# Optimization experiments

Hardware: AMD Instinct MI355X
Metric: run time of the kernel (lower is better)

## Reference

```python
import jax, jax.numpy as jnp
import numpy as np

B, N, D, H = 64, 64, 128, 256
DIN = N + 4        # z_where(2) + one-hot(N) + actions(2)
DOUT = 2
TAU = 0.5
BN_EPS = 1e-5
KL_EPS = 1e-16


def mlp_bn(x, w1, b1, g, bb, w2, b2):
    # Linear -> ReLU -> BatchNorm1d (training mode, stats over all leading dims) -> Linear
    h = jax.nn.relu(jnp.einsum('...i,ih->...h', x, w1) + b1)
    hf = h.reshape(-1, h.shape[-1])
    mu = hf.mean(0)
    var = hf.var(0)  # biased variance, as torch BN uses for normalization
    h = (h - mu) * jax.lax.rsqrt(var + BN_EPS) * g + bb
    return jnp.einsum('...h,ho->...o', h, w2) + b2


def setup_inputs():
    key = jax.random.key(0)
    ks = jax.random.split(key, 16)
    def W(k, i, o):
        return jax.random.normal(k, (i, o), jnp.float32) / np.float32(np.sqrt(i))
    u = jax.random.uniform(ks[0], (B, N, N, 2), jnp.float32, 1e-10, 1.0 - 1e-10)
    gumbel_noise = -jnp.log(-jnp.log(u))
    z = jnp.zeros
    return {
        'states': jax.random.normal(ks[1], (B, N, D), jnp.float32),
        'z_where': jax.random.normal(ks[2], (B, N, 2), jnp.float32),
        'actions': jax.random.normal(ks[3], (B, 2), jnp.float32),
        'gumbel_noise': gumbel_noise,
        'self_w1': W(ks[4], DIN, H), 'self_b1': z((H,)), 'self_g': jnp.ones((H,)), 'self_bb': z((H,)),
        'self_w2': W(ks[5], H, D), 'self_b2': z((D,)),
        'rel_w1': W(ks[6], 2 * D, H), 'rel_b1': z((H,)), 'rel_g': jnp.ones((H,)), 'rel_bb': z((H,)),
        'rel_w2': W(ks[7], H, D), 'rel_b2': z((D,)),
        'wgt_w1': W(ks[8], 2 * D, H), 'wgt_b1': z((H,)), 'wgt_g': jnp.ones((H,)), 'wgt_bb': z((H,)),
        'wgt_w2': W(ks[9], H, 2), 'wgt_b2': z((2,)),
        'pred_w1': W(ks[10], D, H), 'pred_b1': z((H,)), 'pred_g': jnp.ones((H,)), 'pred_bb': z((H,)),
        'pred_w2': W(ks[11], H, DOUT), 'pred_b2': z((DOUT,)),
        'gru_wih': W(ks[12], 2 * D, 3 * D), 'gru_whh': W(ks[13], D, 3 * D),
        'gru_bih': z((3 * D,)), 'gru_bhh': z((3 * D,)),
    }


def prop_gt_forward(states, z_where, actions, gumbel_noise,
                    self_w1, self_b1, self_g, self_bb, self_w2, self_b2,
                    rel_w1, rel_b1, rel_g, rel_bb, rel_w2, rel_b2,
                    wgt_w1, wgt_b1, wgt_g, wgt_bb, wgt_w2, wgt_b2,
                    pred_w1, pred_b1, pred_g, pred_bb, pred_w2, pred_b2,
                    gru_wih, gru_whh, gru_bih, gru_bhh):
    b = states.shape[0]
    eye = jnp.eye(N, dtype=states.dtype)
    # feat = [z_where, one-hot id, broadcast action] : (B, N, DIN)
    z_what = jnp.broadcast_to(eye[None], (b, N, N))
    act = jnp.broadcast_to(actions[:, None, :], (b, N, 2))
    feat = jnp.concatenate([z_where, z_what, act], axis=-1)
    enc_self = mlp_bn(feat, self_w1, self_b1, self_g, self_bb, self_w2, self_b2)  # (B,N,D)

    # recurrent dynamics: pairwise state concat (B, N, N, 2D)
    s_self = jnp.broadcast_to(states[:, :, None, :], (b, N, N, D))
    s_other = jnp.broadcast_to(states[:, None, :, :], (b, N, N, D))
    feat_matrix = jnp.concatenate([s_self, s_other], axis=-1)

    relational = mlp_bn(feat_matrix, rel_w1, rel_b1, rel_g, rel_bb, rel_w2, rel_b2)  # (B,N,N,D)
    logits = mlp_bn(feat_matrix, wgt_w1, wgt_b1, wgt_g, wgt_bb, wgt_w2, wgt_b2)      # (B,N,N,2)

    # gumbel-softmax, hard with straight-through
    y_soft = jax.nn.softmax((logits + gumbel_noise) / TAU, axis=-1)
    y_hard = jax.nn.one_hot(jnp.argmax(y_soft, axis=-1), 2, dtype=y_soft.dtype)
    y = jax.lax.stop_gradient(y_hard - y_soft) + y_soft
    weight = y[..., 0:1]  # (B,N,N,1)

    # KL(prob || prior) as in NRI
    log_prior = jnp.log(jnp.array([0.05, 0.95], dtype=logits.dtype))
    prob = jax.nn.softmax(logits, axis=-1)
    kl_loss = jnp.sum(prob * (jnp.log(prob + KL_EPS) - log_prior)) / (N * b)

    # self mask: zero diagonal edges
    weight = weight * (1.0 - eye)[None, :, :, None]

    enc_rel = jnp.sum(weight * relational, axis=2)  # (B,N,D)

    # TrackerRNN: GRU cell update of states with [enc_self, enc_rel]
    x = jnp.concatenate([enc_self, enc_rel], axis=-1)  # (B,N,2D)
    gi = jnp.einsum('bni,ih->bnh', x, gru_wih) + gru_bih
    gh = jnp.einsum('bnd,dh->bnh', states, gru_whh) + gru_bhh
    gi_r, gi_z, gi_n = jnp.split(gi, 3, axis=-1)
    gh_r, gh_z, gh_n = jnp.split(gh, 3, axis=-1)
    r = jax.nn.sigmoid(gi_r + gh_r)
    zg = jax.nn.sigmoid(gi_z + gh_z)
    n = jnp.tanh(gi_n + r * gh_n)
    updated_state = (1.0 - zg) * n + zg * states  # (B,N,D)

    z_where_next = mlp_bn(updated_state, pred_w1, pred_b1, pred_g, pred_bb, pred_w2, pred_b2)
    return (updated_state, z_where_next.reshape(b, -1), weight, kl_loss)


def reference(states, z_where, actions, gumbel_noise,
              self_w1, self_b1, self_g, self_bb, self_w2, self_b2,
              rel_w1, rel_b1, rel_g, rel_bb, rel_w2, rel_b2,
              wgt_w1, wgt_b1, wgt_g, wgt_bb, wgt_w2, wgt_b2,
              pred_w1, pred_b1, pred_g, pred_bb, pred_w2, pred_b2,
              gru_wih, gru_whh, gru_bih, gru_bhh):
    return prop_gt_forward(states, z_where, actions, gumbel_noise,
                           self_w1, self_b1, self_g, self_bb, self_w2, self_b2,
                           rel_w1, rel_b1, rel_g, rel_bb, rel_w2, rel_b2,
                           wgt_w1, wgt_b1, wgt_g, wgt_bb, wgt_w2, wgt_b2,
                           pred_w1, pred_b1, pred_g, pred_bb, pred_w2, pred_b2,
                           gru_wih, gru_whh, gru_bih, gru_bhh)
```

## Files before the change

kernel.cpp:

```cpp
#include <hip/hip_runtime.h>
#include <math.h>

#define BATCH 64
#define NOBJ  64
#define DDIM  128
#define HDIM  256
#define ROWS  (BATCH*NOBJ)
#define PAIRS (ROWS*NOBJ)

#define OFF_A_REL    (0ull)
#define OFF_B_REL    (4ull<<20)
#define OFF_A_WGT    (8ull<<20)
#define OFF_B_WGT    (12ull<<20)
#define OFF_BWT      (16ull<<20)
#define OFF_H_SELF   (20ull<<20)
#define OFF_ENC_SELF (24ull<<20)
#define OFF_ENC_REL  (26ull<<20)
#define OFF_H_PRED   (28ull<<20)
#define OFF_STATS    (32ull<<20)
#define OFF_KLP      (OFF_STATS + 16384)
#define OFF_W2P      (OFF_STATS + 65536)
#define OFF_C2       (OFF_W2P + 128*1024)
#define OFF_W2PD     (OFF_C2 + 512)
#define OFF_C2W      (OFF_W2PD + 4096)
#define OFF_SW2P     (OFF_C2W + 256)
#define OFF_SC2      (OFF_SW2P + 128*1024)

#define OUT_UPD 0
#define OUT_ZWN (ROWS*DDIM)
#define OUT_WGT (OUT_ZWN + ROWS*2)
#define OUT_KL  (OUT_WGT + PAIRS)

__global__ __launch_bounds__(256) void k_pre(
    const float* __restrict__ states,
    const float* __restrict__ rel_w1, const float* __restrict__ rel_b1,
    const float* __restrict__ wgt_w1, const float* __restrict__ wgt_b1,
    const float* __restrict__ z_where, const float* __restrict__ actions,
    const float* __restrict__ self_w1, const float* __restrict__ self_b1,
    float* __restrict__ A_rel, float* __restrict__ B_rel,
    float* __restrict__ A_wgt, float* __restrict__ B_wgt,
    float* __restrict__ B_wgtT, float* __restrict__ h_self,
    double* __restrict__ stats)
{
    const int t = threadIdx.x;
    const int view = blockIdx.y;
    const int row0 = blockIdx.x * 16;

    if (view == 4) {
        const float w_zw0 = self_w1[0*256+t], w_zw1 = self_w1[1*256+t];
        const float w_a0  = self_w1[66*256+t], w_a1 = self_w1[67*256+t];
        const float bb1 = self_b1[t];
        double sum = 0.0, ssq = 0.0;
        for (int r = 0; r < 16; ++r) {
            const int row = row0 + r;
            const int b = row >> 6, i = row & 63;
            const float zw0 = z_where[row*2], zw1 = z_where[row*2+1];
            const float a0 = actions[b*2], a1 = actions[b*2+1];
            float v = self_w1[(2+i)*256+t] + bb1;
            v = fmaf(zw0, w_zw0, v); v = fmaf(zw1, w_zw1, v);
            v = fmaf(a0, w_a0, v);   v = fmaf(a1, w_a1, v);
            v = fmaxf(v, 0.f);
            h_self[row*256+t] = v;
            sum += (double)v; ssq = fma((double)v, (double)v, ssq);
        }
        atomicAdd(&stats[4*256+t], sum);
        atomicAdd(&stats[5*256+t], ssq);
        return;
    }

    __shared__ float s_tile[16][128];
    for (int f4 = t; f4 < 512; f4 += 256)
        *(float4*)&s_tile[0][f4*4] = *(const float4*)&states[row0*128 + f4*4];
    __syncthreads();

    const float* wbase = (view == 0) ? rel_w1
                       : (view == 1) ? rel_w1 + 128*256
                       : (view == 2) ? wgt_w1
                       :               wgt_w1 + 128*256;
    const float* wp = wbase + t;
    float acc[16];
#pragma unroll
    for (int r = 0; r < 16; ++r) acc[r] = 0.f;
#pragma unroll 4
    for (int k = 0; k < 128; ++k) {
        const float wv = wp[k*256];
#pragma unroll
        for (int r = 0; r < 16; ++r) acc[r] = fmaf(s_tile[r][k], wv, acc[r]);
    }

    if (view == 0) {
        const float bias = rel_b1[t];
#pragma unroll
        for (int r = 0; r < 16; ++r) A_rel[(row0+r)*256 + t] = acc[r] + bias;
    } else if (view == 1) {
#pragma unroll
        for (int r = 0; r < 16; ++r) B_rel[(row0+r)*256 + t] = acc[r];
    } else if (view == 2) {
        const float bias = wgt_b1[t];
#pragma unroll
        for (int r = 0; r < 16; ++r) A_wgt[(row0+r)*256 + t] = acc[r] + bias;
    } else {
#pragma unroll
        for (int r = 0; r < 16; ++r) B_wgt[(row0+r)*256 + t] = acc[r];
        const int b = row0 >> 6, j0 = row0 & 63;
        float* bt = &B_wgtT[((size_t)b*256 + t)*64 + j0];
        *(float4*)(bt+0)  = make_float4(acc[0],  acc[1],  acc[2],  acc[3]);
        *(float4*)(bt+4)  = make_float4(acc[4],  acc[5],  acc[6],  acc[7]);
        *(float4*)(bt+8)  = make_float4(acc[8],  acc[9],  acc[10], acc[11]);
        *(float4*)(bt+12) = make_float4(acc[12], acc[13], acc[14], acc[15]);
    }
}

__global__ __launch_bounds__(256) void k_bn_stats(
    const float* __restrict__ A_rel, const float* __restrict__ B_rel,
    const float* __restrict__ A_wgt, const float* __restrict__ B_wgt,
    double* __restrict__ stats)
{
    const int h = threadIdx.x;
    const int b = blockIdx.y, i0 = blockIdx.x * 8;
    float ar[8], aw[8];
#pragma unroll
    for (int r = 0; r < 8; ++r) {
        ar[r] = A_rel[(b*64 + i0 + r)*256 + h];
        aw[r] = A_wgt[(b*64 + i0 + r)*256 + h];
    }
    float  srel0 = 0.f, ssrel0 = 0.f, srel1 = 0.f, ssrel1 = 0.f;
    double swgt = 0.0, sswgt = 0.0;
    for (int j = 0; j < 64; j += 2) {
        const float br0 = B_rel[(b*64+j)*256 + h];
        const float bw0 = B_wgt[(b*64+j)*256 + h];
        const float br1 = B_rel[(b*64+j+1)*256 + h];
        const float bw1 = B_wgt[(b*64+j+1)*256 + h];
#pragma unroll
        for (int r = 0; r < 8; ++r) {
            const float v0 = fmaxf(ar[r] + br0, 0.f);
            srel0 += v0; ssrel0 = fmaf(v0, v0, ssrel0);
            const float vw0 = fmaxf(aw[r] + bw0, 0.f);
            swgt += (double)vw0; sswgt = fma((double)vw0, (double)vw0, sswgt);
        }
#pragma unroll
        for (int r = 0; r < 8; ++r) {
            const float v1 = fmaxf(ar[r] + br1, 0.f);
            srel1 += v1; ssrel1 = fmaf(v1, v1, ssrel1);
            const float vw1 = fmaxf(aw[r] + bw1, 0.f);
            swgt += (double)vw1; sswgt = fma((double)vw1, (double)vw1, sswgt);
        }
    }
    atomicAdd(&stats[0*256+h], (double)(srel0 + srel1));
    atomicAdd(&stats[1*256+h], (double)(ssrel0 + ssrel1));
    atomicAdd(&stats[2*256+h], swgt);
    atomicAdd(&stats[3*256+h], sswgt);
}

__global__ __launch_bounds__(256) void k_finalize(
    const double* __restrict__ stats,
    const float* __restrict__ rel_g, const float* __restrict__ rel_bb,
    const float* __restrict__ rel_w2, const float* __restrict__ rel_b2,
    const float* __restrict__ wgt_g, const float* __restrict__ wgt_bb,
    const float* __restrict__ wgt_w2, const float* __restrict__ wgt_b2,
    const float* __restrict__ self_g, const float* __restrict__ self_bb,
    const float* __restrict__ self_w2, const float* __restrict__ self_b2,
    float* __restrict__ W2p, float* __restrict__ c2,
    double* __restrict__ W2pd, double* __restrict__ c2w,
    float* __restrict__ sW2p, float* __restrict__ sc2)
{
    __shared__ float  rscale[256], rshift[256], sscale[256], sshift[256];
    __shared__ double wshift[256];
    const int k = threadIdx.x;
    {
        const double cnt = 262144.0;
        double mu  = stats[0*256+k]/cnt;
        double var = stats[1*256+k]/cnt - mu*mu;
        float  sc  = (float)((double)rel_g[k] / sqrt(var + 1e-5));
        rscale[k] = sc;
        rshift[k] = rel_bb[k] - (float)mu * sc;
        double muw  = stats[2*256+k]/cnt;
        double varw = stats[3*256+k]/cnt - muw*muw;
        double scw  = (double)wgt_g[k] / sqrt(varw + 1e-5);
        wshift[k]   = (double)wgt_bb[k] - muw*scw;
        if (blockIdx.x == 0) {
            W2pd[2*k]   = scw * (double)wgt_w2[2*k];
            W2pd[2*k+1] = scw * (double)wgt_w2[2*k+1];
        }
        const double cnts = 4096.0;
        double mus  = stats[4*256+k]/cnts;
        double vars = stats[5*256+k]/cnts - mus*mus;
        float  scs  = (float)((double)self_g[k] / sqrt(vars + 1e-5));
        sscale[k] = scs;
        sshift[k] = self_bb[k] - (float)mus*scs;
    }
    __syncthreads();
    const int base = blockIdx.x * 8192;
    for (int idx = base + k; idx < base + 8192; idx += 256) {
        const int kk = idx >> 7;
        W2p[idx]  = rscale[kk]*rel_w2[idx];
        sW2p[idx] = sscale[kk]*self_w2[idx];
    }
    if (blockIdx.x == 0) {
        if (k < 128) {
            float acc = rel_b2[k], accs = self_b2[k];
            for (int kk = 0; kk < 256; ++kk) {
                acc  = fmaf(rshift[kk], rel_w2[kk*128+k], acc);
                accs = fmaf(sshift[kk], self_w2[kk*128+k], accs);
            }
            c2[k] = acc; sc2[k] = accs;
        }
        if (k < 2) {
            double acc = (double)wgt_b2[k];
            for (int kk = 0; kk < 256; ++kk) acc += wshift[kk]*(double)wgt_w2[kk*2+k];
            c2w[k] = acc;
        }
    }
}

__global__ __launch_bounds__(256) void k_main(
    const float* __restrict__ A_rel, const float* __restrict__ B_rel,
    const float* __restrict__ A_wgt, const float* __restrict__ B_wgtT,
    const double* __restrict__ W2pd, const double* __restrict__ c2w,
    const float* __restrict__ gumbel,
    const float* __restrict__ W2p, const float* __restrict__ c2,
    float* __restrict__ enc_rel, float* __restrict__ weight_out,
    float* __restrict__ klp)
{
    __shared__ float  a_lds[4][256];
    __shared__ double w2_lds[512];
    __shared__ double red0[4][4][64], red1[4][4][64];
    __shared__ float  w_lds[4][64];
    __shared__ float  klred[256];
    __shared__ float  h_lds[4][256];
    __shared__ float  redf[4][256];
    const int t = threadIdx.x;
    const int blk = blockIdx.x;
    const int row0 = blk * 4;
    const int b = row0 >> 6;

    w2_lds[t]     = W2pd[t];
    w2_lds[256+t] = W2pd[256+t];
    float a_rel[4];
#pragma unroll
    for (int r = 0; r < 4; ++r) {
        a_lds[r][t] = A_wgt[(row0+r)*256 + t];
        a_rel[r]    = A_rel[(row0+r)*256 + t];
    }
    __syncthreads();

    {
        const int j = t & 63, q = t >> 6;
        double acc0[4] = {0,0,0,0}, acc1[4] = {0,0,0,0};
        const float* btp = &B_wgtT[((size_t)b*256 + q*64)*64 + j];
#pragma unroll 4
        for (int kk = 0; kk < 64; ++kk) {
            const int k = q*64 + kk;
            const float  bw = btp[kk*64];
            const double w0 = w2_lds[2*k], w1 = w2_lds[2*k+1];
#pragma unroll
            for (int r = 0; r < 4; ++r) {
                const double hw = (double)fmaxf(a_lds[r][k] + bw, 0.f);
                acc0[r] = fma(hw, w0, acc0[r]);
                acc1[r] = fma(hw, w1, acc1[r]);
            }
        }
#pragma unroll
        for (int r = 0; r < 4; ++r) { red0[r][q][j] = acc0[r]; red1[r][q][j] = acc1[r]; }
    }
    __syncthreads();

    {
        const int r = t >> 6, j = t & 63;
        const double l0 = red0[r][0][j]+red0[r][1][j]+red0[r][2][j]+red0[r][3][j] + c2w[0];
        const double l1 = red1[r][0][j]+red1[r][1][j]+red1[r][2][j]+red1[r][3][j] + c2w[1];
        const int row = row0 + r;
        const float g0 = gumbel[(row*64+j)*2], g1 = gumbel[(row*64+j)*2+1];
        float w = (l0 + (double)g0 >= l1 + (double)g1) ? 1.f : 0.f;
        if (j == (row & 63)) w = 0.f;
        w_lds[r][j] = w;
        weight_out[row*64 + j] = w;
        const float lf0 = (float)l0, lf1 = (float)l1;
        const float m = fmaxf(lf0, lf1);
        const float e0 = expf(lf0 - m), e1 = expf(lf1 - m);
        const float s = e0 + e1;
        const float p0 = e0/s, p1 = e1/s;
        const float lp0 = -2.9957323f;
        const float lp1 = -0.05129329f;
        klred[t] = p0*(logf(p0+1e-16f) - lp0) + p1*(logf(p1+1e-16f) - lp1);
    }
    __syncthreads();
    if (t < 64) {
        float s = klred[t] + klred[t+64] + klred[t+128] + klred[t+192];
        for (int off = 32; off; off >>= 1) s += __shfl_down(s, off);
        if (t == 0) klp[blk] = s;
    }

    float sumw[4] = {0,0,0,0};
    {
        float g[4] = {0,0,0,0};
#pragma unroll 4
        for (int j = 0; j < 64; ++j) {
            const float br = B_rel[(b*64+j)*256 + t];
#pragma unroll
            for (int r = 0; r < 4; ++r) {
                const float w = w_lds[r][j];
                sumw[r] += w;
                g[r] = fmaf(w, fmaxf(a_rel[r] + br, 0.f), g[r]);
            }
        }
#pragma unroll
        for (int r = 0; r < 4; ++r) h_lds[r][t] = g[r];
    }
    __syncthreads();
    {
        const int d = t & 127, half = t >> 7;
        float acc[4] = {0,0,0,0};
        const float* wp = &W2p[half*128*128 + d];
#pragma unroll 2
        for (int kk = 0; kk < 128; ++kk) {
            const float wv = wp[kk*128];
#pragma unroll
            for (int r = 0; r < 4; ++r)
                acc[r] = fmaf(h_lds[r][half*128 + kk], wv, acc[r]);
        }
#pragma unroll
        for (int r = 0; r < 4; ++r) redf[r][t] = acc[r];
    }
    __syncthreads();
    if (t < 128) {
#pragma unroll
        for (int r = 0; r < 4; ++r)
            enc_rel[(row0+r)*128 + t] = redf[r][t] + redf[r][t+128] + sumw[r]*c2[t];
    }
}

__global__ __launch_bounds__(256) void k_enc_self(
    const float* __restrict__ h_self, const float* __restrict__ sW2p,
    const float* __restrict__ sc2, float* __restrict__ enc_self)
{
    __shared__ float h_lds[16*256];
    const int t = threadIdx.x;
    const int row0 = blockIdx.x * 16;
    for (int f4 = t; f4 < 1024; f4 += 256)
        *(float4*)&h_lds[f4*4] = *(const float4*)&h_self[row0*256 + f4*4];
    __syncthreads();
    const int d = t & 127, half = t >> 7;
    float acc[16];
#pragma unroll
    for (int r = 0; r < 16; ++r) acc[r] = 0.f;
    for (int kk = 0; kk < 128; ++kk) {
        const int k = half*128 + kk;
        const float wv = sW2p[k*128 + d];
#pragma unroll
        for (int r = 0; r < 16; ++r) acc[r] = fmaf(h_lds[r*256 + k], wv, acc[r]);
    }
    __syncthreads();
#pragma unroll
    for (int r = 0; r < 16; ++r) h_lds[r*256 + t] = acc[r];
    __syncthreads();
    for (int idx = t; idx < 16*128; idx += 256) {
        const int r = idx >> 7, dd = idx & 127;
        enc_self[(row0+r)*128 + dd] = h_lds[r*256 + dd] + h_lds[r*256 + 128 + dd] + sc2[dd];
    }
}

__global__ __launch_bounds__(384) void k_gru(
    const float* __restrict__ enc_self, const float* __restrict__ enc_rel,
    const float* __restrict__ states,
    const float* __restrict__ wih, const float* __restrict__ whh,
    const float* __restrict__ bih, const float* __restrict__ bhh,
    float* __restrict__ updated)
{
    __shared__ float x_lds[8][256];
    __shared__ float s_lds[8][128];
    __shared__ float gi_lds[8][384];
    __shared__ float gh_lds[8][384];
    const int t = threadIdx.x;
    const int row0 = blockIdx.x * 8;
    for (int idx = t; idx < 8*256; idx += 384) {
        const int r = idx >> 8, k = idx & 255;
        x_lds[r][k] = (k < 128) ? enc_self[(row0+r)*128 + k]
                                : enc_rel[(row0+r)*128 + (k-128)];
    }
    for (int idx = t; idx < 8*128; idx += 384) {
        const int r = idx >> 7, k = idx & 127;
        s_lds[r][k] = states[(row0+r)*128 + k];
    }
    __syncthreads();
    float gi[8], gh[8];
    const float bi = bih[t], bh = bhh[t];
#pragma unroll
    for (int r = 0; r < 8; ++r) { gi[r] = bi; gh[r] = bh; }
    for (int k = 0; k < 256; ++k) {
        const float w = wih[k*384 + t];
#pragma unroll
        for (int r = 0; r < 8; ++r) gi[r] = fmaf(x_lds[r][k], w, gi[r]);
    }
    for (int k = 0; k < 128; ++k) {
        const float w = whh[k*384 + t];
#pragma unroll
        for (int r = 0; r < 8; ++r) gh[r] = fmaf(s_lds[r][k], w, gh[r]);
    }
#pragma unroll
    for (int r = 0; r < 8; ++r) { gi_lds[r][t] = gi[r]; gh_lds[r][t] = gh[r]; }
    __syncthreads();
    for (int idx = t; idx < 8*128; idx += 384) {
        const int r = idx >> 7, d = idx & 127;
        const float gr = gi_lds[r][d]       + gh_lds[r][d];
        const float gz = gi_lds[r][128+d]   + gh_lds[r][128+d];
        const float rr = 1.f/(1.f + expf(-gr));
        const float zz = 1.f/(1.f + expf(-gz));
        const float nn = tanhf(gi_lds[r][256+d] + rr*gh_lds[r][256+d]);
        updated[(row0+r)*128 + d] = (1.f - zz)*nn + zz*s_lds[r][d];
    }
}

__global__ __launch_bounds__(256) void k_pred_h(
    const float* __restrict__ updated, const float* __restrict__ w1,
    const float* __restrict__ b1, float* __restrict__ h_pred,
    double* __restrict__ stats)
{
    __shared__ float u_lds[16][128];
    const int h = threadIdx.x;
    const int row0 = blockIdx.x * 16;
    for (int f4 = h; f4 < 512; f4 += 256)
        *(float4*)&u_lds[0][f4*4] = *(const float4*)&updated[row0*128 + f4*4];
    __syncthreads();
    float acc[16];
    const float bb1 = b1[h];
#pragma unroll
    for (int r = 0; r < 16; ++r) acc[r] = bb1;
#pragma unroll 4
    for (int k = 0; k < 128; ++k) {
        const float w = w1[k*256 + h];
#pragma unroll
        for (int r = 0; r < 16; ++r) acc[r] = fmaf(u_lds[r][k], w, acc[r]);
    }
    double sum = 0.0, ssq = 0.0;
#pragma unroll
    for (int r = 0; r < 16; ++r) {
        const float v = fmaxf(acc[r], 0.f);
        h_pred[(row0+r)*256 + h] = v;
        sum += (double)v; ssq = fma((double)v, (double)v, ssq);
    }
    atomicAdd(&stats[6*256+h], sum);
    atomicAdd(&stats[7*256+h], ssq);
}

__global__ __launch_bounds__(256) void k_pred_out(
    const float* __restrict__ h_pred, const double* __restrict__ stats,
    const float* __restrict__ g, const float* __restrict__ bbv,
    const float* __restrict__ w2, const float* __restrict__ b2,
    const float* __restrict__ klp,
    float* __restrict__ out_zw, float* __restrict__ out_kl)
{
    __shared__ float scale_lds[256], shift_lds[256];
    __shared__ float h_lds[32*256];
    __shared__ float red0[256], red1[256];
    __shared__ double kred[4];
    const int t = threadIdx.x;
    {
        const double mu  = stats[6*256+t]/4096.0;
        const double var = stats[7*256+t]/4096.0 - mu*mu;
        const float  sc  = (float)((double)g[t]/sqrt(var + 1e-5));
        scale_lds[t] = sc;
        shift_lds[t] = bbv[t] - (float)mu*sc;
    }
    const int row0 = blockIdx.x * 32;
    for (int idx = t; idx < 32*256; idx += 256)
        h_lds[idx] = h_pred[row0*256 + idx];
    __syncthreads();
    const int rl = t >> 3, q = t & 7;
    float a0 = 0.f, a1 = 0.f;
    for (int kk = 0; kk < 32; ++kk) {
        const int k = q*32 + kk;
        const float hn = fmaf(h_lds[rl*256 + k], scale_lds[k], shift_lds[k]);
        a0 = fmaf(hn, w2[k*2],   a0);
        a1 = fmaf(hn, w2[k*2+1], a1);
    }
    red0[t] = a0; red1[t] = a1;
    __syncthreads();
    if (t < 32) {
        float z0 = b2[0], z1 = b2[1];
        for (int q2 = 0; q2 < 8; ++q2) { z0 += red0[t*8+q2]; z1 += red1[t*8+q2]; }
        out_zw[(row0+t)*2]   = z0;
        out_zw[(row0+t)*2+1] = z1;
    }
    if (blockIdx.x == 0) {
        double s = 0.0;
        for (int idx = t; idx < 1024; idx += 256) s += (double)klp[idx];
        for (int off = 32; off; off >>= 1) s += __shfl_down(s, off);
        if ((t & 63) == 0) kred[t >> 6] = s;
        __syncthreads();
        if (t == 0)
            out_kl[0] = (float)((kred[0]+kred[1]+kred[2]+kred[3]) / 4096.0);
    }
}

extern "C" void kernel_launch(void* const* d_in, const int* in_sizes, int n_in,
                              void* d_out, int out_size, void* d_ws, size_t ws_size,
                              hipStream_t stream) {
    const float* states   = (const float*)d_in[0];
    const float* z_where  = (const float*)d_in[1];
    const float* actions  = (const float*)d_in[2];
    const float* gumbel   = (const float*)d_in[3];
    const float* self_w1  = (const float*)d_in[4];
    const float* self_b1  = (const float*)d_in[5];
    const float* self_g   = (const float*)d_in[6];
    const float* self_bb  = (const float*)d_in[7];
    const float* self_w2  = (const float*)d_in[8];
    const float* self_b2  = (const float*)d_in[9];
    const float* rel_w1   = (const float*)d_in[10];
    const float* rel_b1   = (const float*)d_in[11];
    const float* rel_g    = (const float*)d_in[12];
    const float* rel_bb   = (const float*)d_in[13];
    const float* rel_w2   = (const float*)d_in[14];
    const float* rel_b2   = (const float*)d_in[15];
    const float* wgt_w1   = (const float*)d_in[16];
    const float* wgt_b1   = (const float*)d_in[17];
    const float* wgt_g    = (const float*)d_in[18];
    const float* wgt_bb   = (const float*)d_in[19];
    const float* wgt_w2   = (const float*)d_in[20];
    const float* wgt_b2   = (const float*)d_in[21];
    const float* pred_w1  = (const float*)d_in[22];
    const float* pred_b1  = (const float*)d_in[23];
    const float* pred_g   = (const float*)d_in[24];
    const float* pred_bb  = (const float*)d_in[25];
    const float* pred_w2  = (const float*)d_in[26];
    const float* pred_b2  = (const float*)d_in[27];
    const float* gru_wih  = (const float*)d_in[28];
    const float* gru_whh  = (const float*)d_in[29];
    const float* gru_bih  = (const float*)d_in[30];
    const float* gru_bhh  = (const float*)d_in[31];

    char* ws = (char*)d_ws;
    float*  A_rel  = (float*) (ws + OFF_A_REL);
    float*  B_rel  = (float*) (ws + OFF_B_REL);
    float*  A_wgt  = (float*) (ws + OFF_A_WGT);
    float*  B_wgt  = (float*) (ws + OFF_B_WGT);
    float*  B_wgtT = (float*) (ws + OFF_BWT);
    float*  h_self = (float*) (ws + OFF_H_SELF);
    float*  encS   = (float*) (ws + OFF_ENC_SELF);
    float*  encR   = (float*) (ws + OFF_ENC_REL);
    float*  h_pred = (float*) (ws + OFF_H_PRED);
    double* stats  = (double*)(ws + OFF_STATS);
    float*  klp    = (float*) (ws + OFF_KLP);
    float*  W2p    = (float*) (ws + OFF_W2P);
    float*  c2     = (float*) (ws + OFF_C2);
    double* W2pd   = (double*)(ws + OFF_W2PD);
    double* c2w    = (double*)(ws + OFF_C2W);
    float*  sW2p   = (float*) (ws + OFF_SW2P);
    float*  sc2    = (float*) (ws + OFF_SC2);

    float* out = (float*)d_out;

    hipMemsetAsync(ws + OFF_STATS, 0, 8*256*8, stream);

    k_pre<<<dim3(256, 5), 256, 0, stream>>>(states, rel_w1, rel_b1, wgt_w1, wgt_b1,
                                            z_where, actions, self_w1, self_b1,
                                            A_rel, B_rel, A_wgt, B_wgt, B_wgtT,
                                            h_self, stats);
    k_bn_stats<<<dim3(8, 64), 256, 0, stream>>>(A_rel, B_rel, A_wgt, B_wgt, stats);
    k_finalize<<<4, 256, 0, stream>>>(stats, rel_g, rel_bb, rel_w2, rel_b2,
                                      wgt_g, wgt_bb, wgt_w2, wgt_b2,
                                      self_g, self_bb, self_w2, self_b2,
                                      W2p, c2, W2pd, c2w, sW2p, sc2);
    k_main<<<1024, 256, 0, stream>>>(A_rel, B_rel, A_wgt, B_wgtT, W2pd, c2w,
                                     gumbel, W2p, c2, encR, out + OUT_WGT, klp);
    k_enc_self<<<256, 256, 0, stream>>>(h_self, sW2p, sc2, encS);
    k_gru<<<512, 384, 0, stream>>>(encS, encR, states, gru_wih, gru_whh,
                                   gru_bih, gru_bhh, out + OUT_UPD);
    k_pred_h<<<256, 256, 0, stream>>>(out + OUT_UPD, pred_w1, pred_b1, h_pred, stats);
    k_pred_out<<<128, 256, 0, stream>>>(h_pred, stats, pred_g, pred_bb, pred_w2, pred_b2,
                                        klp, out + OUT_ZWN, out + OUT_KL);
}
```

Before: 202.5 us.

## Retile GRU kernel so each thread computes all three gates for a 2x2 output tile

Rewrites the GRU kernel so each of 256 threads owns 2 rows by 2 columns and accumulates the r, z and n gates directly in registers, merging the r/z input and hidden sums. This removes the intermediate gi/gh shared-memory arrays and the second barrier. Global loads become float4 and float2 vectorised. Weight loads are now float2 per gate at strides of 384, and each thread holds more accumulators in registers.

Measured after the change: 231.7 us. 1.14x slower.

```diff
diff --git a/kernel.cpp b/kernel.cpp
--- a/kernel.cpp
+++ b/kernel.cpp
@@ -360,54 +360,108 @@
     }
 }
 
-__global__ __launch_bounds__(384) void k_gru(
+__global__ __launch_bounds__(256) void k_gru(
     const float* __restrict__ enc_self, const float* __restrict__ enc_rel,
     const float* __restrict__ states,
     const float* __restrict__ wih, const float* __restrict__ whh,
     const float* __restrict__ bih, const float* __restrict__ bhh,
     float* __restrict__ updated)
 {
-    __shared__ float x_lds[8][256];
-    __shared__ float s_lds[8][128];
-    __shared__ float gi_lds[8][384];
-    __shared__ float gh_lds[8][384];
+    __shared__ float x_lds[8][384];
     const int t = threadIdx.x;
     const int row0 = blockIdx.x * 8;
-    for (int idx = t; idx < 8*256; idx += 384) {
-        const int r = idx >> 8, k = idx & 255;
-        x_lds[r][k] = (k < 128) ? enc_self[(row0+r)*128 + k]
-                                : enc_rel[(row0+r)*128 + (k-128)];
-    }
-    for (int idx = t; idx < 8*128; idx += 384) {
-        const int r = idx >> 7, k = idx & 127;
-        s_lds[r][k] = states[(row0+r)*128 + k];
-    }
-    __syncthreads();
-    float gi[8], gh[8];
-    const float bi = bih[t], bh = bhh[t];
-#pragma unroll
-    for (int r = 0; r < 8; ++r) { gi[r] = bi; gh[r] = bh; }
-    for (int k = 0; k < 256; ++k) {
-        const float w = wih[k*384 + t];
-#pragma unroll
-        for (int r = 0; r < 8; ++r) gi[r] = fmaf(x_lds[r][k], w, gi[r]);
-    }
-    for (int k = 0; k < 128; ++k) {
-        const float w = whh[k*384 + t];
-#pragma unroll
-        for (int r = 0; r < 8; ++r) gh[r] = fmaf(s_lds[r][k], w, gh[r]);
-    }
-#pragma unroll
-    for (int r = 0; r < 8; ++r) { gi_lds[r][t] = gi[r]; gh_lds[r][t] = gh[r]; }
-    __syncthreads();
-    for (int idx = t; idx < 8*128; idx += 384) {
-        const int r = idx >> 7, d = idx & 127;
-        const float gr = gi_lds[r][d]       + gh_lds[r][d];
-        const float gz = gi_lds[r][128+d]   + gh_lds[r][128+d];
-        const float rr = 1.f/(1.f + expf(-gr));
-        const float zz = 1.f/(1.f + expf(-gz));
-        const float nn = tanhf(gi_lds[r][256+d] + rr*gh_lds[r][256+d]);
-        updated[(row0+r)*128 + d] = (1.f - zz)*nn + zz*s_lds[r][d];
+    {
+        const int r = t >> 5, q = (t & 31) * 4;
+        *(float4*)&x_lds[r][q]       = *(const float4*)&enc_self[(row0+r)*128 + q];
+        *(float4*)&x_lds[r][128+q]   = *(const float4*)&enc_rel [(row0+r)*128 + q];
+        *(float4*)&x_lds[r][256+q]   = *(const float4*)&states  [(row0+r)*128 + q];
+    }
+    __syncthreads();
+
+    const int c0 = t & 63;
+    const int rg = t >> 6;
+    const int d0 = c0 * 2;
+    const int r0 = rg * 2;
+
+    float ar[2][2], az[2][2], agin[2][2], aghn[2][2];
+    {
+        const float2 bi_r = *(const float2*)&bih[d0];
+        const float2 bi_z = *(const float2*)&bih[128+d0];
+        const float2 bi_n = *(const float2*)&bih[256+d0];
+        const float2 bh_r = *(const float2*)&bhh[d0];
+        const float2 bh_z = *(const float2*)&bhh[128+d0];
+        const float2 bh_n = *(const float2*)&bhh[256+d0];
+#pragma unroll
+        for (int m = 0; m < 2; ++m) {
+            ar[m][0] = bi_r.x + bh_r.x;  ar[m][1] = bi_r.y + bh_r.y;
+            az[m][0] = bi_z.x + bh_z.x;  az[m][1] = bi_z.y + bh_z.y;
+            agin[m][0] = bi_n.x;         agin[m][1] = bi_n.y;
+            aghn[m][0] = bh_n.x;         aghn[m][1] = bh_n.y;
+        }
+    }
+
+    {
+        const float* wp = wih + d0;
+        for (int k0 = 0; k0 < 256; k0 += 4) {
+            const float4 xa = *(const float4*)&x_lds[r0][k0];
+            const float4 xb = *(const float4*)&x_lds[r0+1][k0];
+            const float xm[2][4] = {{xa.x, xa.y, xa.z, xa.w}, {xb.x, xb.y, xb.z, xb.w}};
+#pragma unroll
+            for (int kk = 0; kk < 4; ++kk) {
+                const float2 wr = *(const float2*)&wp[(k0+kk)*384];
+                const float2 wz = *(const float2*)&wp[(k0+kk)*384 + 128];
+                const float2 wn = *(const float2*)&wp[(k0+kk)*384 + 256];
+#pragma unroll
+                for (int m = 0; m < 2; ++m) {
+                    const float x = xm[m][kk];
+                    ar[m][0]   = fmaf(x, wr.x, ar[m][0]);
+                    ar[m][1]   = fmaf(x, wr.y, ar[m][1]);
+                    az[m][0]   = fmaf(x, wz.x, az[m][0]);
+                    az[m][1]   = fmaf(x, wz.y, az[m][1]);
+                    agin[m][0] = fmaf(x, wn.x, agin[m][0]);
+                    agin[m][1] = fmaf(x, wn.y, agin[m][1]);
+                }
+            }
+        }
+    }
+    {
+        const float* wp = whh + d0;
+        for (int k0 = 0; k0 < 128; k0 += 4) {
+            const float4 xa = *(const float4*)&x_lds[r0][256 + k0];
+            const float4 xb = *(const float4*)&x_lds[r0+1][256 + k0];
+            const float xm[2][4] = {{xa.x, xa.y, xa.z, xa.w}, {xb.x, xb.y, xb.z, xb.w}};
+#pragma unroll
+            for (int kk = 0; kk < 4; ++kk) {
+                const float2 wr = *(const float2*)&wp[(k0+kk)*384];
+                const float2 wz = *(const float2*)&wp[(k0+kk)*384 + 128];
+                const float2 wn = *(const float2*)&wp[(k0+kk)*384 + 256];
+#pragma unroll
+                for (int m = 0; m < 2; ++m) {
+                    const float x = xm[m][kk];
+                    ar[m][0]   = fmaf(x, wr.x, ar[m][0]);
+                    ar[m][1]   = fmaf(x, wr.y, ar[m][1]);
+                    az[m][0]   = fmaf(x, wz.x, az[m][0]);
+                    az[m][1]   = fmaf(x, wz.y, az[m][1]);
+                    aghn[m][0] = fmaf(x, wn.x, aghn[m][0]);
+                    aghn[m][1] = fmaf(x, wn.y, aghn[m][1]);
+                }
+            }
+        }
+    }
+
+#pragma unroll
+    for (int m = 0; m < 2; ++m) {
+        const int row = row0 + r0 + m;
+        float out[2];
+#pragma unroll
+        for (int e = 0; e < 2; ++e) {
+            const float rr = 1.f / (1.f + expf(-ar[m][e]));
+            const float zz = 1.f / (1.f + expf(-az[m][e]));
+            const float nn = tanhf(agin[m][e] + rr * aghn[m][e]);
+            const float s  = x_lds[r0+m][256 + d0 + e];
+            out[e] = (1.f - zz) * nn + zz * s;
+        }
+        *(float2*)&updated[row*128 + d0] = make_float2(out[0], out[1]);
     }
 }
 
@@ -564,7 +618,7 @@
     k_main<<<1024, 256, 0, stream>>>(A_rel, B_rel, A_wgt, B_wgtT, W2pd, c2w,
                                      gumbel, W2p, c2, encR, out + OUT_WGT, klp);
     k_enc_self<<<256, 256, 0, stream>>>(h_self, sW2p, sc2, encS);
-    k_gru<<<512, 384, 0, stream>>>(encS, encR, states, gru_wih, gru_whh,
+    k_gru<<<512, 256, 0, stream>>>(encS, encR, states, gru_wih, gru_whh,
                                    gru_bih, gru_bhh, out + OUT_UPD);
     k_pred_h<<<256, 256, 0, stream>>>(out + OUT_UPD, pred_w1, pred_b1, h_pred, stats);
     k_pred_out<<<128, 256, 0, stream>>>(h_pred, stats, pred_g, pred_bb, pred_w2, pred_b2,
```
